# Kernel tuning notes

Hardware: AMD Instinct MI355X
Metric: run time of the kernel (lower is better)

Reference implementation:

```python
import jax, jax.numpy as jnp
import numpy as np

HEADS = 8
DIM_HEAD = 64
WIN = 16
DIM = 256
INNER = HEADS * DIM_HEAD  # 512
SCALE = DIM_HEAD ** -0.5


def _to_windows(t, heads, w):
    # 'b (h c) (X w1) (Y w2) -> (b h X Y) (w1 w2) c'
    b, hc, H, W = t.shape
    c = hc // heads
    X, Y = H // w, W // w
    t = t.reshape(b, heads, c, X, w, Y, w)
    t = t.transpose(0, 1, 3, 5, 4, 6, 2)  # b h X Y w1 w2 c
    return t.reshape(b * heads * X * Y, w * w, c)


def _from_windows(t, b, heads, H, W, w):
    # '(b h X Y) (w1 w2) c -> b (h c) (X w1) (Y w2)'
    X, Y = H // w, W // w
    c = t.shape[-1]
    t = t.reshape(b, heads, X, Y, w, w, c)
    t = t.transpose(0, 1, 6, 2, 4, 3, 5)  # b h c X w1 Y w2
    return t.reshape(b, heads * c, H, W)


def setup_inputs() -> dict:
    key = jax.random.key(0)
    k1, k2, k3, k4 = jax.random.split(key, 4)
    x = jax.random.normal(k1, (4, DIM, 128, 128), dtype=jnp.float32)
    Wq = jax.random.normal(k2, (INNER, DIM), dtype=jnp.float32) * 0.02
    Wkv = jax.random.normal(k3, (2 * INNER, DIM), dtype=jnp.float32) * 0.02
    Wo = jax.random.normal(k4, (DIM, INNER), dtype=jnp.float32) * 0.02
    bo = jnp.zeros((DIM,), dtype=jnp.float32)
    return {"x": x, "Wq": Wq, "Wkv": Wkv, "Wo": Wo, "bo": bo}


def reference(x, Wq, Wkv, Wo, bo):
    b, _, H, W = x.shape
    # 1x1 convs == channel matmuls
    q = jnp.einsum('oc,bchw->bohw', Wq, x)
    kv = jnp.einsum('oc,bchw->bohw', Wkv, x)
    k, v = jnp.split(kv, 2, axis=1)
    q = _to_windows(q, HEADS, WIN)
    k = _to_windows(k, HEADS, WIN)
    v = _to_windows(v, HEADS, WIN)
    sim = jnp.einsum('bid,bjd->bij', q, k) * SCALE
    attn = jax.nn.softmax(sim, axis=-1)
    out = jnp.einsum('bij,bjd->bid', attn, v)
    out = _from_windows(out, b, HEADS, H, W, WIN)
    return jnp.einsum('oc,bchw->bohw', Wo, out) + bo[None, :, None, None]
```

## Files before the change

kernel.cpp:

```cpp
#include <hip/hip_runtime.h>
#include <stdint.h>

typedef unsigned short u16;
typedef short bf16x8 __attribute__((ext_vector_type(8)));
typedef float f32x4 __attribute__((ext_vector_type(4)));
typedef u16 u16x8 __attribute__((ext_vector_type(8)));
typedef u16 u16x4 __attribute__((ext_vector_type(4)));
typedef uint32_t u32x4 __attribute__((ext_vector_type(4)));
typedef uint32_t u32x2 __attribute__((ext_vector_type(2)));

typedef const __attribute__((address_space(1))) void gvoid_t;
typedef __attribute__((address_space(3))) void lvoid_t;

__device__ __forceinline__ u16 f2bf(float f) {
  uint32_t u = __float_as_uint(f);
  return (u16)((u + 0x7fffu + ((u >> 16) & 1u)) >> 16);
}

__device__ __forceinline__ uint32_t cvtpk(float a, float b) {
  uint32_t r;
  asm("v_cvt_pk_bf16_f32 %0, %1, %2" : "=v"(r) : "v"(a), "v"(b));
  return r;
}

__device__ __forceinline__ void gload16(const void* g, void* l) {
  __builtin_amdgcn_global_load_lds((gvoid_t*)g, (lvoid_t*)l, 16, 0, 0);
}

__global__ __launch_bounds__(256) void k_convert_w(
    const float* __restrict__ Wq, const float* __restrict__ Wkv,
    const float* __restrict__ Wo, u16* __restrict__ Wcat, u16* __restrict__ Wobf) {
  const int i = blockIdx.x * 256 + threadIdx.x;
  if (i < 131072) {
    Wcat[i] = f2bf(Wq[i]);
  } else if (i < 393216) {
    Wcat[i] = f2bf(Wkv[i - 131072]);
  } else {
    Wobf[i - 393216] = f2bf(Wo[i - 393216]);
  }
}

__global__ __launch_bounds__(256) void k_convert_x(
    const float* __restrict__ x, u16* __restrict__ xbT) {
  const int p = blockIdx.x * 256 + threadIdx.x;
  const int b = p >> 14, hw = p & 16383;
  const float* src = x + ((size_t)b << 22) + hw;
  u16* dst = xbT + ((size_t)p << 8);
  for (int c0 = 0; c0 < 256; c0 += 8) {
    u16x8 v;
#pragma unroll
    for (int j = 0; j < 8; ++j)
      v[j] = f2bf(src[(size_t)(c0 + j) << 14]);
    *(u16x8*)(dst + c0) = v;
  }
}

template <int KTOT, int MODE>
__global__ __launch_bounds__(512) void k_gemm(
    const u16* __restrict__ A, const u16* __restrict__ B,
    u16* __restrict__ qws, u16* __restrict__ kws, u16* __restrict__ vws,
    float* __restrict__ dout, const float* __restrict__ bo) {
  __shared__ __align__(16) char As[2][16384];
  __shared__ __align__(16) char Bs[2][16384];
  const int tid = threadIdx.x;
  const int lane = tid & 63, wid = tid >> 6;
  const int wr = wid & 1, wc = wid >> 1;
  const int l15 = lane & 15, lg = lane >> 4;
  const int MT = (MODE == 0) ? 12 : 2;
  const int nwgPerXcd = (MODE == 0) ? 768 : 128;
  const int bid = (blockIdx.x & 7) * nwgPerXcd + (blockIdx.x >> 3);
  const int mt = bid % MT, nt = bid / MT;
  const int m0 = mt * 128, n0 = nt * 128;
  constexpr int NT = KTOT / 64;

  auto stage = [&](int buf, int k0) {
#pragma unroll
    for (int c = 0; c < 2; ++c) {
      const int u = c * 512 + tid;
      const int row = u >> 3;
      const int sb = ((u & 7) * 16) ^ ((row & 7) << 4);
      gload16((const char*)A + ((size_t)(m0 + row) * KTOT + k0) * 2 + sb,
              As[buf] + u * 16);
      if constexpr (MODE == 0) {
        gload16((const char*)B + ((size_t)(n0 + row) * KTOT + k0) * 2 + sb,
                Bs[buf] + u * 16);
      } else {
        const int col = n0 + row;
        const int b = col >> 14, hw = col & 16383;
        const int h = hw >> 7, w = hw & 127;
        const int token = ((h & 15) << 4) | (w & 15);
        const int whb = (b << 9) + ((h >> 4) << 3) + (w >> 4);
        const int cch = k0 + (sb >> 1);
        gload16(B + ((size_t)whb << 14) + ((size_t)(cch >> 6) << 20) +
                    token * 64 + (cch & 63),
                Bs[buf] + u * 16);
      }
    }
  };

  f32x4 acc[4][2] = {};

  stage(0, 0);
  int cur = 0;
  for (int t = 0; t < NT; ++t) {
    if (t + 1 < NT) {
      stage(cur ^ 1, (t + 1) * 64);
      asm volatile("s_waitcnt vmcnt(4)" ::: "memory");
    } else {
      asm volatile("s_waitcnt vmcnt(0)" ::: "memory");
    }
    __builtin_amdgcn_s_barrier();
    const char* Ab = As[cur];
    const char* Bb = Bs[cur];
#pragma unroll
    for (int kk = 0; kk < 2; ++kk) {
      bf16x8 af[4], bfr[2];
#pragma unroll
      for (int t4 = 0; t4 < 4; ++t4) {
        const int ra = wr * 64 + t4 * 16 + l15;
        af[t4] = *(const bf16x8*)(Ab + ra * 128 + ((kk * 64 + lg * 16) ^ ((ra & 7) << 4)));
      }
#pragma unroll
      for (int t2 = 0; t2 < 2; ++t2) {
        const int rb = wc * 32 + t2 * 16 + l15;
        bfr[t2] = *(const bf16x8*)(Bb + rb * 128 + ((kk * 64 + lg * 16) ^ ((rb & 7) << 4)));
      }
      __builtin_amdgcn_s_setprio(1);
#pragma unroll
      for (int i = 0; i < 4; ++i)
#pragma unroll
        for (int jj = 0; jj < 2; ++jj)
          acc[i][jj] = __builtin_amdgcn_mfma_f32_16x16x32_bf16(af[i], bfr[jj], acc[i][jj], 0, 0, 0);
      __builtin_amdgcn_s_setprio(0);
    }
    __builtin_amdgcn_s_barrier();
    cur ^= 1;
  }

  if (MODE == 0) {
    u16* dst = (m0 < 512) ? qws : (m0 < 1024) ? kws : vws;
    const bool isv = (m0 >= 1024);
    if (!isv) {
#pragma unroll
      for (int ct = 0; ct < 2; ++ct) {
        const int col = n0 + wc * 32 + ct * 16 + l15;
        const int b = col >> 14, hw = col & 16383;
        const int h = hw >> 7, w = hw & 127;
        const int token = ((h & 15) << 4) | (w & 15);
        const int npart = (((b << 9) + ((h >> 4) << 3) + (w >> 4)) << 14) + token * 64;
#pragma unroll
        for (int rt = 0; rt < 4; ++rt) {
          const int mm = (m0 + wr * 64 + rt * 16 + lg * 4) & 511;
          const int head = mm >> 6, d = mm & 63;
          u16x4 pk;
#pragma unroll
          for (int r = 0; r < 4; ++r) pk[r] = f2bf(acc[rt][ct][r]);
          *(u16x4*)(dst + (size_t)(npart + (head << 20) + d)) = pk;
        }
      }
    } else {
#pragma unroll
      for (int ct = 0; ct < 2; ++ct) {
        const int col = n0 + wc * 32 + ct * 16 + l15;
        const int b = col >> 14, hw = col & 16383;
        const int h = hw >> 7, w = hw & 127;
        const int token = ((h & 15) << 4) | (w & 15);
        const int npart = (((b << 9) + ((h >> 4) << 3) + (w >> 4)) << 14) + token;
#pragma unroll
        for (int rt = 0; rt < 4; ++rt)
#pragma unroll
          for (int r = 0; r < 4; ++r) {
            const int mm = (m0 + wr * 64 + rt * 16 + lg * 4 + r) & 511;
            const int head = mm >> 6, d = mm & 63;
            dst[(size_t)(npart + (head << 20) + (d << 8))] = f2bf(acc[rt][ct][r]);
          }
      }
    }
  } else {
#pragma unroll
    for (int rt = 0; rt < 4; ++rt)
#pragma unroll
      for (int r = 0; r < 4; ++r) {
        const int o = m0 + wr * 64 + rt * 16 + lg * 4 + r;
        const float bias = bo[o];
#pragma unroll
        for (int ct = 0; ct < 2; ++ct) {
          const int col = n0 + wc * 32 + ct * 16 + l15;
          const int b = col >> 14, hw = col & 16383;
          dout[(((size_t)(b << 8) + o) << 14) + hw] = acc[rt][ct][r] + bias;
        }
      }
  }
}

__global__ __launch_bounds__(512, 4) void k_attn(
    const u16* __restrict__ qws, const u16* __restrict__ kws,
    const u16* __restrict__ vws, u16* __restrict__ aout) {
  __shared__ __align__(16) u16 Ks[16384];
  __shared__ __align__(16) u16 Vs[16384];
  const int tid = threadIdx.x, lane = tid & 63, wid = tid >> 6;
  const int l15 = lane & 15, lg = lane >> 4;
  const int wh = blockIdx.x;
  const u16* qb = qws + ((size_t)wh << 14);
  const char* kbc = (const char*)(kws + ((size_t)wh << 14));
  const char* vbc = (const char*)(vws + ((size_t)wh << 14));
  u16* ob = aout + ((size_t)wh << 14);

  bf16x8 qf[2][2];
#pragma unroll
  for (int chunk = 0; chunk < 2; ++chunk)
#pragma unroll
    for (int kk = 0; kk < 2; ++kk)
      qf[chunk][kk] = *(const bf16x8*)(qb + (wid * 32 + chunk * 16 + l15) * 64 +
                                       kk * 32 + lg * 8);

#pragma unroll
  for (int pass = 0; pass < 4; ++pass) {
    const int o = pass * 8192 + tid * 16;
    {
      const int row = o >> 7, c = o & 127;
      gload16(kbc + row * 128 + (c ^ ((row & 7) << 4)), (char*)Ks + o);
    }
    {
      const int row = o >> 9, c = o & 511;
      gload16(vbc + row * 512 + (c ^ ((row & 7) << 4)), (char*)Vs + o);
    }
  }
  __syncthreads();

  const int idxA = ((lg & 1) << 5) + l15;
  const int idxB = idxA + 16;
  const bool useY = (lg & 2) != 0;
  const float cexp = 0.125f * 1.44269504088896f;

  f32x4 o4[2][4] = {};
  f32x4 sum4[2] = {};

#pragma unroll
  for (int h = 0; h < 2; ++h) {
#pragma unroll
    for (int chunk = 0; chunk < 2; ++chunk) {
      f32x4 s[8] = {};
      __builtin_amdgcn_s_setprio(1);
#pragma unroll
      for (int kk = 0; kk < 2; ++kk)
#pragma unroll
        for (int ct = 0; ct < 8; ++ct) {
          const int krow = h * 128 + ct * 16 + l15;
          bf16x8 kf = *(const bf16x8*)((const char*)Ks + krow * 128 +
                                       ((kk * 64 + lg * 16) ^ ((krow & 7) << 4)));
          s[ct] = __builtin_amdgcn_mfma_f32_16x16x32_bf16(kf, qf[chunk][kk], s[ct], 0, 0, 0);
        }
      __builtin_amdgcn_s_setprio(0);

#pragma unroll
      for (int ct = 0; ct < 8; ++ct) {
#pragma unroll
        for (int r = 0; r < 4; ++r) s[ct][r] = exp2f(s[ct][r] * cexp);
        sum4[chunk] += s[ct];
      }

      int pkLo[8], pkHi[8];
#pragma unroll
      for (int ct = 0; ct < 8; ++ct) {
        pkLo[ct] = (int)cvtpk(s[ct][0], s[ct][1]);
        pkHi[ct] = (int)cvtpk(s[ct][2], s[ct][3]);
      }

#pragma unroll
      for (int kt = 0; kt < 4; ++kt) {
        const int ev = 2 * kt, od = 2 * kt + 1;
        int xa0 = __shfl(pkLo[ev], idxA), xa1 = __shfl(pkHi[ev], idxA);
        int xb0 = __shfl(pkLo[ev], idxB), xb1 = __shfl(pkHi[ev], idxB);
        int ya0 = __shfl(pkLo[od], idxA), ya1 = __shfl(pkHi[od], idxA);
        int yb0 = __shfl(pkLo[od], idxB), yb1 = __shfl(pkHi[od], idxB);
        u32x4 w;
        w[0] = (uint32_t)(useY ? ya0 : xa0);
        w[1] = (uint32_t)(useY ? ya1 : xa1);
        w[2] = (uint32_t)(useY ? yb0 : xb0);
        w[3] = (uint32_t)(useY ? yb1 : xb1);
        bf16x8 pf = __builtin_bit_cast(bf16x8, w);
        __builtin_amdgcn_s_setprio(1);
#pragma unroll
        for (int dt = 0; dt < 4; ++dt) {
          const int vrow = dt * 16 + l15;
          bf16x8 vf = *(const bf16x8*)((const char*)Vs + vrow * 512 +
                                       ((h * 256 + kt * 64 + lg * 16) ^ ((vrow & 7) << 4)));
          o4[chunk][dt] = __builtin_amdgcn_mfma_f32_16x16x32_bf16(vf, pf, o4[chunk][dt], 0, 0, 0);
        }
        __builtin_amdgcn_s_setprio(0);
      }
    }
  }

#pragma unroll
  for (int chunk = 0; chunk < 2; ++chunk) {
    const int tok = wid * 32 + chunk * 16 + l15;
    float hs = (sum4[chunk][0] + sum4[chunk][1]) + (sum4[chunk][2] + sum4[chunk][3]);
    hs += __shfl_xor(hs, 16);
    hs += __shfl_xor(hs, 32);
    const float pinv = 1.0f / hs;
#pragma unroll
    for (int dt = 0; dt < 4; ++dt) {
      u32x2 pk;
      pk[0] = cvtpk(o4[chunk][dt][0] * pinv, o4[chunk][dt][1] * pinv);
      pk[1] = cvtpk(o4[chunk][dt][2] * pinv, o4[chunk][dt][3] * pinv);
      *(u32x2*)(ob + tok * 64 + dt * 16 + lg * 4) = pk;
    }
  }
}

extern "C" void kernel_launch(void* const* d_in, const int* in_sizes, int n_in,
                              void* d_out, int out_size, void* d_ws, size_t ws_size,
                              hipStream_t stream) {
  const float* x   = (const float*)d_in[0];
  const float* Wq  = (const float*)d_in[1];
  const float* Wkv = (const float*)d_in[2];
  const float* Wo  = (const float*)d_in[3];
  const float* bo  = (const float*)d_in[4];
  float* out = (float*)d_out;

  char* ws = (char*)d_ws;
  u16* xbT  = (u16*)ws;
  u16* Wcat = (u16*)(ws + 33554432);
  u16* Wobf = (u16*)(ws + 34340864);
  u16* kws  = (u16*)(ws + 34603008);
  u16* vws  = (u16*)(ws + 101711872);
  u16* qws  = (u16*)d_out;

  k_convert_w<<<2048, 256, 0, stream>>>(Wq, Wkv, Wo, Wcat, Wobf);
  k_convert_x<<<256, 256, 0, stream>>>(x, xbT);
  k_gemm<256, 0><<<6144, 512, 0, stream>>>(Wcat, xbT, qws, kws, vws, nullptr, nullptr);
  k_attn<<<2048, 512, 0, stream>>>(qws, kws, vws, kws);
  k_gemm<512, 1><<<1024, 512, 0, stream>>>(Wobf, kws, nullptr, nullptr, nullptr, out, bo);
}
```

Before: 237.2 us.

## Replace generic QKV GEMM with per-window-head kernel loading operands directly

Replaces the LDS-staged, double-buffered 128x128 GEMM for the QKV projection with a kernel where each block computes Q, K and V for one (window, head) pair. Operands come straight from global memory into registers with no LDS and no barriers, and each x fragment is shared across the three projections. The epilogue writes directly in the windowed layout with simpler index math. The trade-off is that weight fragments are reloaded from global/L2 by every block and there is no software pipelining of loads, so the kernel may become latency-bound. The per-element transposed V store remains.

```diff
diff --git a/kernel.cpp b/kernel.cpp
--- a/kernel.cpp
+++ b/kernel.cpp
@@ -55,141 +55,67 @@
   }
 }
 
-template <int KTOT, int MODE>
-__global__ __launch_bounds__(512) void k_gemm(
-    const u16* __restrict__ A, const u16* __restrict__ B,
-    u16* __restrict__ qws, u16* __restrict__ kws, u16* __restrict__ vws,
-    float* __restrict__ dout, const float* __restrict__ bo) {
-  __shared__ __align__(16) char As[2][16384];
-  __shared__ __align__(16) char Bs[2][16384];
-  const int tid = threadIdx.x;
-  const int lane = tid & 63, wid = tid >> 6;
-  const int wr = wid & 1, wc = wid >> 1;
+__global__ __launch_bounds__(512) void k_qkv(
+    const u16* __restrict__ Wcat, const u16* __restrict__ xbT,
+    u16* __restrict__ qws, u16* __restrict__ kws, u16* __restrict__ vws) {
+  const int tid = threadIdx.x, lane = tid & 63, wid = tid >> 6;
   const int l15 = lane & 15, lg = lane >> 4;
-  const int MT = (MODE == 0) ? 12 : 2;
-  const int nwgPerXcd = (MODE == 0) ? 768 : 128;
-  const int bid = (blockIdx.x & 7) * nwgPerXcd + (blockIdx.x >> 3);
-  const int mt = bid % MT, nt = bid / MT;
-  const int m0 = mt * 128, n0 = nt * 128;
-  constexpr int NT = KTOT / 64;
-
-  auto stage = [&](int buf, int k0) {
-#pragma unroll
-    for (int c = 0; c < 2; ++c) {
-      const int u = c * 512 + tid;
-      const int row = u >> 3;
-      const int sb = ((u & 7) * 16) ^ ((row & 7) << 4);
-      gload16((const char*)A + ((size_t)(m0 + row) * KTOT + k0) * 2 + sb,
-              As[buf] + u * 16);
-      if constexpr (MODE == 0) {
-        gload16((const char*)B + ((size_t)(n0 + row) * KTOT + k0) * 2 + sb,
-                Bs[buf] + u * 16);
-      } else {
-        const int col = n0 + row;
-        const int b = col >> 14, hw = col & 16383;
-        const int h = hw >> 7, w = hw & 127;
-        const int token = ((h & 15) << 4) | (w & 15);
-        const int whb = (b << 9) + ((h >> 4) << 3) + (w >> 4);
-        const int cch = k0 + (sb >> 1);
-        gload16(B + ((size_t)whb << 14) + ((size_t)(cch >> 6) << 20) +
-                    token * 64 + (cch & 63),
-                Bs[buf] + u * 16);
-      }
-    }
-  };
-
-  f32x4 acc[4][2] = {};
-
-  stage(0, 0);
-  int cur = 0;
-  for (int t = 0; t < NT; ++t) {
-    if (t + 1 < NT) {
-      stage(cur ^ 1, (t + 1) * 64);
-      asm volatile("s_waitcnt vmcnt(4)" ::: "memory");
-    } else {
-      asm volatile("s_waitcnt vmcnt(0)" ::: "memory");
-    }
-    __builtin_amdgcn_s_barrier();
-    const char* Ab = As[cur];
-    const char* Bb = Bs[cur];
-#pragma unroll
-    for (int kk = 0; kk < 2; ++kk) {
-      bf16x8 af[4], bfr[2];
-#pragma unroll
-      for (int t4 = 0; t4 < 4; ++t4) {
-        const int ra = wr * 64 + t4 * 16 + l15;
-        af[t4] = *(const bf16x8*)(Ab + ra * 128 + ((kk * 64 + lg * 16) ^ ((ra & 7) << 4)));
-      }
-#pragma unroll
-      for (int t2 = 0; t2 < 2; ++t2) {
-        const int rb = wc * 32 + t2 * 16 + l15;
-        bfr[t2] = *(const bf16x8*)(Bb + rb * 128 + ((kk * 64 + lg * 16) ^ ((rb & 7) << 4)));
-      }
-      __builtin_amdgcn_s_setprio(1);
-#pragma unroll
-      for (int i = 0; i < 4; ++i)
-#pragma unroll
-        for (int jj = 0; jj < 2; ++jj)
-          acc[i][jj] = __builtin_amdgcn_mfma_f32_16x16x32_bf16(af[i], bfr[jj], acc[i][jj], 0, 0, 0);
-      __builtin_amdgcn_s_setprio(0);
-    }
-    __builtin_amdgcn_s_barrier();
-    cur ^= 1;
-  }
-
-  if (MODE == 0) {
-    u16* dst = (m0 < 512) ? qws : (m0 < 1024) ? kws : vws;
-    const bool isv = (m0 >= 1024);
-    if (!isv) {
-#pragma unroll
-      for (int ct = 0; ct < 2; ++ct) {
-        const int col = n0 + wc * 32 + ct * 16 + l15;
-        const int b = col >> 14, hw = col & 16383;
-        const int h = hw >> 7, w = hw & 127;
-        const int token = ((h & 15) << 4) | (w & 15);
-        const int npart = (((b << 9) + ((h >> 4) << 3) + (w >> 4)) << 14) + token * 64;
-#pragma unroll
-        for (int rt = 0; rt < 4; ++rt) {
-          const int mm = (m0 + wr * 64 + rt * 16 + lg * 4) & 511;
-          const int head = mm >> 6, d = mm & 63;
-          u16x4 pk;
-#pragma unroll
-          for (int r = 0; r < 4; ++r) pk[r] = f2bf(acc[rt][ct][r]);
-          *(u16x4*)(dst + (size_t)(npart + (head << 20) + d)) = pk;
+  const int bw = (blockIdx.x & 7) * 256 + (blockIdx.x >> 3);
+  const int head = bw & 7, wlin = bw >> 3;
+  const int b = wlin >> 6, X = (wlin >> 3) & 7, Y = wlin & 7;
+  const int wh = (b << 9) + (head << 6) + (X << 3) + Y;
+
+  f32x4 aq[4][2] = {}, ak[4][2] = {}, av[4][2] = {};
+  const char* xb = (const char*)xbT;
+  const char* wb = (const char*)Wcat;
+  const int rq = head * 64, rk = 512 + head * 64, rv = 1024 + head * 64;
+#pragma unroll
+  for (int half = 0; half < 2; ++half) {
+#pragma unroll
+    for (int kk = 0; kk < 4; ++kk) {
+      const int cb = half * 256 + kk * 64 + lg * 16;
+      bf16x8 bx[2];
+#pragma unroll
+      for (int tt = 0; tt < 2; ++tt) {
+        const int pix = (b << 14) + (X << 11) + (wid * 2 + tt) * 128 + (Y << 4) + l15;
+        bx[tt] = *(const bf16x8*)(xb + (size_t)pix * 512 + cb);
+      }
+#pragma unroll
+      for (int dt = 0; dt < 4; ++dt) {
+        bf16x8 wqf = *(const bf16x8*)(wb + (size_t)(rq + dt * 16 + l15) * 512 + cb);
+        bf16x8 wkf = *(const bf16x8*)(wb + (size_t)(rk + dt * 16 + l15) * 512 + cb);
+        bf16x8 wvf = *(const bf16x8*)(wb + (size_t)(rv + dt * 16 + l15) * 512 + cb);
+#pragma unroll
+        for (int tt = 0; tt < 2; ++tt) {
+          aq[dt][tt] = __builtin_amdgcn_mfma_f32_16x16x32_bf16(wqf, bx[tt], aq[dt][tt], 0, 0, 0);
+          ak[dt][tt] = __builtin_amdgcn_mfma_f32_16x16x32_bf16(wkf, bx[tt], ak[dt][tt], 0, 0, 0);
+          av[dt][tt] = __builtin_amdgcn_mfma_f32_16x16x32_bf16(wvf, bx[tt], av[dt][tt], 0, 0, 0);
         }
       }
-    } else {
-#pragma unroll
-      for (int ct = 0; ct < 2; ++ct) {
-        const int col = n0 + wc * 32 + ct * 16 + l15;
-        const int b = col >> 14, hw = col & 16383;
-        const int h = hw >> 7, w = hw & 127;
-        const int token = ((h & 15) << 4) | (w & 15);
-        const int npart = (((b << 9) + ((h >> 4) << 3) + (w >> 4)) << 14) + token;
-#pragma unroll
-        for (int rt = 0; rt < 4; ++rt)
-#pragma unroll
-          for (int r = 0; r < 4; ++r) {
-            const int mm = (m0 + wr * 64 + rt * 16 + lg * 4 + r) & 511;
-            const int head = mm >> 6, d = mm & 63;
-            dst[(size_t)(npart + (head << 20) + (d << 8))] = f2bf(acc[rt][ct][r]);
-          }
-      }
-    }
-  } else {
-#pragma unroll
-    for (int rt = 0; rt < 4; ++rt)
+    }
+  }
+
+  u16* qb = qws + ((size_t)wh << 14);
+  u16* kb = kws + ((size_t)wh << 14);
+  u16* vb = vws + ((size_t)wh << 14);
+#pragma unroll
+  for (int tt = 0; tt < 2; ++tt) {
+    const int tok = wid * 32 + tt * 16 + l15;
+#pragma unroll
+    for (int dt = 0; dt < 4; ++dt) {
+      const int d = dt * 16 + lg * 4;
+      u16x4 pq, pk;
 #pragma unroll
       for (int r = 0; r < 4; ++r) {
-        const int o = m0 + wr * 64 + rt * 16 + lg * 4 + r;
-        const float bias = bo[o];
-#pragma unroll
-        for (int ct = 0; ct < 2; ++ct) {
-          const int col = n0 + wc * 32 + ct * 16 + l15;
-          const int b = col >> 14, hw = col & 16383;
-          dout[(((size_t)(b << 8) + o) << 14) + hw] = acc[rt][ct][r] + bias;
-        }
-      }
+        pq[r] = f2bf(aq[dt][tt][r]);
+        pk[r] = f2bf(ak[dt][tt][r]);
+      }
+      *(u16x4*)(qb + tok * 64 + d) = pq;
+      *(u16x4*)(kb + tok * 64 + d) = pk;
+#pragma unroll
+      for (int r = 0; r < 4; ++r)
+        vb[(d + r) * 256 + tok] = f2bf(av[dt][tt][r]);
+    }
   }
 }
 
@@ -310,6 +236,97 @@
   }
 }
 
+template <int KTOT, int MODE>
+__global__ __launch_bounds__(512) void k_gemm(
+    const u16* __restrict__ A, const u16* __restrict__ B,
+    float* __restrict__ dout, const float* __restrict__ bo) {
+  __shared__ __align__(16) char As[2][16384];
+  __shared__ __align__(16) char Bs[2][16384];
+  const int tid = threadIdx.x;
+  const int lane = tid & 63, wid = tid >> 6;
+  const int wr = wid & 1, wc = wid >> 1;
+  const int l15 = lane & 15, lg = lane >> 4;
+  const int MT = 2;
+  const int nwgPerXcd = 128;
+  const int bid = (blockIdx.x & 7) * nwgPerXcd + (blockIdx.x >> 3);
+  const int mt = bid % MT, nt = bid / MT;
+  const int m0 = mt * 128, n0 = nt * 128;
+  constexpr int NT = KTOT / 64;
+
+  auto stage = [&](int buf, int k0) {
+#pragma unroll
+    for (int c = 0; c < 2; ++c) {
+      const int u = c * 512 + tid;
+      const int row = u >> 3;
+      const int sb = ((u & 7) * 16) ^ ((row & 7) << 4);
+      gload16((const char*)A + ((size_t)(m0 + row) * KTOT + k0) * 2 + sb,
+              As[buf] + u * 16);
+      const int col = n0 + row;
+      const int b = col >> 14, hw = col & 16383;
+      const int h = hw >> 7, w = hw & 127;
+      const int token = ((h & 15) << 4) | (w & 15);
+      const int whb = (b << 9) + ((h >> 4) << 3) + (w >> 4);
+      const int cch = k0 + (sb >> 1);
+      gload16(B + ((size_t)whb << 14) + ((size_t)(cch >> 6) << 20) +
+                  token * 64 + (cch & 63),
+              Bs[buf] + u * 16);
+    }
+  };
+
+  f32x4 acc[4][2] = {};
+
+  stage(0, 0);
+  int cur = 0;
+  for (int t = 0; t < NT; ++t) {
+    if (t + 1 < NT) {
+      stage(cur ^ 1, (t + 1) * 64);
+      asm volatile("s_waitcnt vmcnt(4)" ::: "memory");
+    } else {
+      asm volatile("s_waitcnt vmcnt(0)" ::: "memory");
+    }
+    __builtin_amdgcn_s_barrier();
+    const char* Ab = As[cur];
+    const char* Bb = Bs[cur];
+#pragma unroll
+    for (int kk = 0; kk < 2; ++kk) {
+      bf16x8 af[4], bfr[2];
+#pragma unroll
+      for (int t4 = 0; t4 < 4; ++t4) {
+        const int ra = wr * 64 + t4 * 16 + l15;
+        af[t4] = *(const bf16x8*)(Ab + ra * 128 + ((kk * 64 + lg * 16) ^ ((ra & 7) << 4)));
+      }
+#pragma unroll
+      for (int t2 = 0; t2 < 2; ++t2) {
+        const int rb = wc * 32 + t2 * 16 + l15;
+        bfr[t2] = *(const bf16x8*)(Bb + rb * 128 + ((kk * 64 + lg * 16) ^ ((rb & 7) << 4)));
+      }
+      __builtin_amdgcn_s_setprio(1);
+#pragma unroll
+      for (int i = 0; i < 4; ++i)
+#pragma unroll
+        for (int jj = 0; jj < 2; ++jj)
+          acc[i][jj] = __builtin_amdgcn_mfma_f32_16x16x32_bf16(af[i], bfr[jj], acc[i][jj], 0, 0, 0);
+      __builtin_amdgcn_s_setprio(0);
+    }
+    __builtin_amdgcn_s_barrier();
+    cur ^= 1;
+  }
+
+#pragma unroll
+  for (int rt = 0; rt < 4; ++rt)
+#pragma unroll
+    for (int r = 0; r < 4; ++r) {
+      const int o = m0 + wr * 64 + rt * 16 + lg * 4 + r;
+      const float bias = bo[o];
+#pragma unroll
+      for (int ct = 0; ct < 2; ++ct) {
+        const int col = n0 + wc * 32 + ct * 16 + l15;
+        const int b = col >> 14, hw = col & 16383;
+        dout[(((size_t)(b << 8) + o) << 14) + hw] = acc[rt][ct][r] + bias;
+      }
+    }
+}
+
 extern "C" void kernel_launch(void* const* d_in, const int* in_sizes, int n_in,
                               void* d_out, int out_size, void* d_ws, size_t ws_size,
                               hipStream_t stream) {
@@ -330,7 +347,7 @@
 
   k_convert_w<<<2048, 256, 0, stream>>>(Wq, Wkv, Wo, Wcat, Wobf);
   k_convert_x<<<256, 256, 0, stream>>>(x, xbT);
-  k_gemm<256, 0><<<6144, 512, 0, stream>>>(Wcat, xbT, qws, kws, vws, nullptr, nullptr);
+  k_qkv<<<2048, 512, 0, stream>>>(Wcat, xbT, qws, kws, vws);
   k_attn<<<2048, 512, 0, stream>>>(qws, kws, vws, kws);
-  k_gemm<512, 1><<<1024, 512, 0, stream>>>(Wobf, kws, nullptr, nullptr, nullptr, out, bo);
-}
+  k_gemm<512, 1><<<1024, 512, 0, stream>>>(Wobf, kws, out, bo);
+}
```

After: 385.8 us. +62.7%, slower.
